# Kernel tuning notes

Hardware: AMD Instinct MI355X
Metric: run time of the kernel (lower is better)

Reference implementation:

```python
import jax, jax.numpy as jnp
import numpy as np

B, S, H = 8, 2048, 1024   # batch, seq, hidden_size
E = 4                     # num_experts (world_size=1 -> all local)
C = 1024                  # kv_cache_size (cache_decrement=0 -> uniform pyramid)
R = 4                     # LoRA rank
ALPHA = 1.0
TOP_K = 2
TEMP = 1.0
KEEP = C // 2             # pyramid compressor keeps top-half by importance


def _lora(z, A, Bm):
    # LoRALayer: (z @ A) @ B scaled by alpha/rank
    return (z @ A) @ Bm * (ALPHA / A.shape[-1])


def setup_inputs() -> dict:
    key = jax.random.key(0)
    ks = jax.random.split(key, 24)
    w = lambda k, shp: jax.random.normal(k, shp, jnp.float32) * 0.02
    return {
        'x': jax.random.normal(ks[0], (B, S, H), jnp.float32),
        'query': jax.random.normal(ks[1], (B, S, H), jnp.float32),
        'Wg': w(ks[2], (H, E)), 'bg': jnp.zeros((E,), jnp.float32),
        'Wq': w(ks[3], (H, H)), 'bq': jnp.zeros((H,), jnp.float32),
        'Wk': w(ks[4], (H, H)), 'bk': jnp.zeros((H,), jnp.float32),
        'Aq': w(ks[5], (H, R)), 'Bq': w(ks[6], (R, H)),
        'Ak': w(ks[7], (H, R)), 'Bk': w(ks[8], (R, H)),
        'We': w(ks[9], (E, H, H)), 'be': jnp.zeros((E, H), jnp.float32),
        'Ae': w(ks[10], (E, H, R)), 'Be': w(ks[11], (E, R, H)),
        'Av': w(ks[12], (E, H, R)), 'Bv': w(ks[13], (E, R, H)),
        'cache_keys': jax.random.normal(ks[14], (E, C, H), jnp.float32),
        'cache_values': jax.random.normal(ks[15], (E, C, H), jnp.float32),
        'cache_imp': jax.random.uniform(ks[16], (E, C), jnp.float32),
    }


def reference(x, query, Wg, bg, Wq, bq, Wk, bk, Aq, Bq, Ak, Bk,
              We, be, Ae, Be, Av, Bv, cache_keys, cache_values, cache_imp):
    # ---- AdaptiveRouter: softmax gate, top-2 renormalized, load-balance loss ----
    probs = jax.nn.softmax((x @ Wg + bg) / TEMP, axis=-1)             # [B,S,E]
    tw, ti = jax.lax.top_k(probs, TOP_K)                              # [B,S,K]
    twn = tw / tw.sum(-1, keepdims=True)
    onehot = jax.nn.one_hot(ti, E, dtype=x.dtype)                     # [B,S,K,E]
    routing = jnp.einsum('bsk,bske->bse', twn, onehot)                # [B,S,E]
    lb_loss = E * jnp.sum(probs.mean((0, 1)) * onehot.mean((0, 1, 2)))

    # ---- compute_token_importance (query provided): LoRA-augmented q/k attention ----
    q = query @ Wq + bq + _lora(query, Aq, Bq)
    k = x @ Wk + bk + _lora(x, Ak, Bk)
    att = jax.nn.softmax(jnp.einsum('bqh,bkh->bqk', q, k) / np.sqrt(H).astype(np.float32), axis=-1)
    importance = att.sum(axis=1)                                      # [B,S] column sums

    # ---- per-expert LoRA forward + pyramid-compressed cache read ----
    def expert_fn(We_i, be_i, Ae_i, Be_i, Av_i, Bv_i, cv_i, ci_i):
        eo = x @ We_i + be_i + _lora(x, Ae_i, Be_i)                   # [B,S,H]
        idx = jax.lax.top_k(ci_i, KEEP)[1]                            # keep top-half by importance
        vals = cv_i[idx]                                              # [KEEP,H] irregular gather
        vals = vals + _lora(vals, Av_i, Bv_i)                         # value LoRA on compressed cache
        return eo + jax.lax.stop_gradient(vals.mean(0))               # cached values are detached

    outs = jax.vmap(expert_fn)(We, be, Ae, Be, Av, Bv, cache_values, cache_imp)  # [E,B,S,H]
    expert_output = jnp.einsum('ebsh,bse->bsh', outs, routing)

    # ---- cache update at ptr=0 (detached buffer mutation -> returned new state) ----
    sg = jax.lax.stop_gradient
    new_keys = cache_keys.at[:, 0].set(jnp.broadcast_to(sg(x.mean((0, 1))), (E, H)))
    new_values = cache_values.at[:, 0].set(sg(outs.mean((1, 2))))
    new_imp = cache_imp.at[:, 0].set(sg(importance.mean()))
    return expert_output, lb_loss, new_keys, new_values, new_imp
```

## Files before the change

kernel.cpp:

```cpp
#include <hip/hip_runtime.h>

constexpr int kH    = 1024;
constexpr int kNT   = 16384;
constexpr int kE    = 4;
constexpr int kC    = 1024;
constexpr int kR    = 4;
constexpr int kKeep = 512;
constexpr float kLoraScale = 0.25f;
constexpr int kCapTiles = 136;
constexpr int kCapRows  = kCapTiles * 128;
constexpr int kNB      = kNT / 256;

constexpr size_t WS_RW     = 0;
constexpr size_t WS_G      = 65536;
constexpr size_t WS_XSUM   = 393216;
constexpr size_t WS_SHADOW = 394240;
constexpr size_t WS_TU     = 394752;
constexpr size_t WS_VBAR   = 394784;
constexpr size_t WS_FX     = 398880;
constexpr size_t WS_NEWV0  = 402976;
constexpr size_t WS_MSK    = 407072;
constexpr size_t WS_GBASE  = 411168;
constexpr size_t WS_BHIST  = 411176;
constexpr size_t WS_BOFF   = 411560;
constexpr size_t WS_RTPID  = 411944;
constexpr size_t WS_TPID   = 412088;
constexpr size_t WS_GRO    = 428472;
constexpr size_t WS_PERM   = 444856;
constexpr size_t WS_WCAT   = 462264;
constexpr size_t WS_AEXT   = 482744;
constexpr size_t WS_AEXTG  = 744888;
constexpr size_t WS_BEXT   = 1023416;
constexpr size_t WS_WET    = 1039800;
constexpr size_t WS_XG     = 3136952;

constexpr size_t OUT_LB = 16777216;
constexpr size_t OUT_NK = 16777217;

typedef __attribute__((ext_vector_type(8))) short bf16x8;
typedef __attribute__((ext_vector_type(4))) float f32x4;

__device__ __forceinline__ float wred(float v) {
#pragma unroll
  for (int off = 32; off; off >>= 1) v += __shfl_xor(v, off);
  return v;
}

__device__ __forceinline__ ushort f2bf(float f) {
  unsigned int u = __float_as_uint(f);
  u += 0x7FFFu + ((u >> 16) & 1u);
  return (ushort)(u >> 16);
}

__device__ __forceinline__ void gload16(const ushort* g, ushort* l) {
  __builtin_amdgcn_global_load_lds(
      (const __attribute__((address_space(1))) unsigned int*)g,
      (__attribute__((address_space(3))) unsigned int*)l, 16, 0, 0);
}

__device__ __forceinline__ int pid_a(int pid) { return pid < 3 ? 0 : (pid < 5 ? 1 : 2); }
__device__ __forceinline__ int pid_b(int pid) { return pid < 3 ? pid + 1 : (pid < 5 ? pid - 1 : 3); }

__global__ __launch_bounds__(256) void prep_k(const float* __restrict__ Wg,
                                              const float* __restrict__ Ae,
                                              const float* __restrict__ ci,
                                              float* __restrict__ wcat,
                                              float* __restrict__ msk) {
  __shared__ float imp[kC];
  const int b = blockIdx.x, tid = threadIdx.x;
  if (b < 80) {
    const int idx = b * 256 + tid;
    const int c = idx >> 10, k = idx & 1023;
    float v;
    if (c < 4) v = Wg[(size_t)k * 4 + c];
    else {
      const int e = (c - 4) >> 2, r = (c - 4) & 3;
      v = Ae[((size_t)e * kH + k) * kR + r];
    }
    wcat[(size_t)c * kH + k] = v;
  } else {
    const int e = (b - 80) >> 2, part = (b - 80) & 3;
    const int c = part * 256 + tid;
    for (int i = tid; i < kC; i += 256) imp[i] = ci[(size_t)e * kC + i];
    __syncthreads();
    const float v = imp[c];
    int rank = 0;
    for (int c2 = 0; c2 < kC; ++c2) {
      const float v2 = imp[c2];
      rank += (v2 > v) || (v2 == v && c2 < c);
    }
    msk[(size_t)e * kC + c] = (rank < kKeep) ? 1.0f : 0.0f;
  }
}

__global__ __launch_bounds__(256) void router_gemm_k(
    const float* __restrict__ x, const float* __restrict__ wcat,
    float* __restrict__ G) {
  __shared__ float xs_l[128][64];
  __shared__ float wt_l[20][64];
  const int tid = threadIdx.x;
  const int t0 = blockIdx.x * 128;
  const int tok = tid & 127, half = tid >> 7, cb = half * 10;
  float acc[10] = {};
  for (int kc = 0; kc < 16; ++kc) {
#pragma unroll
    for (int i = 0; i < 8; ++i) {
      const int idx = tid + i * 256;
      const int stok = idx >> 4, sslot = idx & 15;
      const float4 v =
          *(const float4*)(x + (size_t)(t0 + stok) * kH + kc * 64 + sslot * 4);
      *(float4*)&xs_l[stok][((sslot + stok) & 15) * 4] = v;
    }
    for (int idx = tid; idx < 320; idx += 256) {
      const int c = idx >> 4, slot = idx & 15;
      *(float4*)&wt_l[c][slot * 4] =
          *(const float4*)(wcat + (size_t)c * kH + kc * 64 + slot * 4);
    }
    __syncthreads();
#pragma unroll
    for (int k4 = 0; k4 < 16; ++k4) {
      const float4 xv = *(const float4*)&xs_l[tok][((k4 + tok) & 15) * 4];
#pragma unroll
      for (int j = 0; j < 10; ++j) {
        const float4 wv = *(const float4*)&wt_l[cb + j][k4 * 4];
        acc[j] += xv.x * wv.x + xv.y * wv.y + xv.z * wv.z + xv.w * wv.w;
      }
    }
    __syncthreads();
  }
#pragma unroll
  for (int j = 0; j < 10; ++j)
    G[(size_t)(cb + j) * kNT + t0 + tok] = acc[j];
}

__global__ __launch_bounds__(256) void router_fin_k(
    const float* __restrict__ G, const float* __restrict__ bg,
    float* __restrict__ rw, float* __restrict__ shadow,
    int* __restrict__ tpid, int* __restrict__ bhist,
    ushort* __restrict__ aext) {
  __shared__ float swacc[8];
  __shared__ int ihist[6];
  const int tid = threadIdx.x;
  const int t = blockIdx.x * 256 + tid;
  const int lane = tid & 63;
  if (tid < 8) swacc[tid] = 0.f;
  if (tid < 6) ihist[tid] = 0;
  __syncthreads();
  float lg[kE];
#pragma unroll
  for (int e = 0; e < kE; ++e) lg[e] = G[(size_t)e * kNT + t] + bg[e];
  float la[kE][kR];
#pragma unroll
  for (int e = 0; e < kE; ++e)
#pragma unroll
    for (int r = 0; r < kR; ++r)
      la[e][r] = G[(size_t)(4 + e * 4 + r) * kNT + t];
  const float mx = fmaxf(fmaxf(lg[0], lg[1]), fmaxf(lg[2], lg[3]));
  float ex[kE], se = 0.f;
#pragma unroll
  for (int e = 0; e < kE; ++e) { ex[e] = __expf(lg[e] - mx); se += ex[e]; }
  float pr[kE];
#pragma unroll
  for (int e = 0; e < kE; ++e) pr[e] = ex[e] / se;
  int e1 = 0;
#pragma unroll
  for (int e = 1; e < kE; ++e) if (pr[e] > pr[e1]) e1 = e;
  int e2 = (e1 == 0) ? 1 : 0;
#pragma unroll
  for (int e = 0; e < kE; ++e) if (e != e1 && pr[e] > pr[e2]) e2 = e;
  const float s2 = pr[e1] + pr[e2];
  float rwv[kE] = {0.f, 0.f, 0.f, 0.f};
  rwv[e1] = pr[e1] / s2; rwv[e2] = pr[e2] / s2;
  *(float4*)(rw + (size_t)t * kE) = make_float4(rwv[0], rwv[1], rwv[2], rwv[3]);
  const int lo = min(e1, e2), hi = max(e1, e2);
  const int pid = (lo == 0) ? hi - 1 : ((lo == 1) ? hi + 1 : 5);
  tpid[t] = pid;
  __align__(16) ushort o[32];
#pragma unroll
  for (int e = 0; e < kE; ++e) o[e] = f2bf(rwv[e]);
#pragma unroll
  for (int e = 0; e < kE; ++e)
#pragma unroll
    for (int r = 0; r < kR; ++r)
      o[4 + e * 4 + r] = f2bf(kLoraScale * rwv[e] * la[e][r]);
#pragma unroll
  for (int i = 20; i < 32; ++i) o[i] = 0;
#pragma unroll
  for (int q = 0; q < 4; ++q)
    *(float4*)&aext[(size_t)t * 32 + q * 8] = *(float4*)&o[q * 8];
  float vals[8];
#pragma unroll
  for (int e = 0; e < kE; ++e) {
    vals[e] = pr[e];
    vals[4 + e] = ((e == e1) ? 1.f : 0.f) + ((e == e2) ? 1.f : 0.f);
  }
#pragma unroll
  for (int j = 0; j < 8; ++j) {
    vals[j] = wred(vals[j]);
    if (lane == 0) atomicAdd(&swacc[j], vals[j]);
  }
  atomicAdd(&ihist[pid], 1);
  __syncthreads();
  if (tid < 8) atomicAdd(&shadow[(blockIdx.x & 63) * 8 + tid], swacc[tid]);
  if (tid < 6) bhist[blockIdx.x * 6 + tid] = ihist[tid];
}

__global__ __launch_bounds__(256) void colsum_k(const float* __restrict__ x,
                                                float* __restrict__ xsum) {
  const int rg = blockIdx.x, tid = threadIdx.x;
  const float* xp = x + (size_t)rg * 64 * kH + tid * 4;
  float s0 = 0.f, s1 = 0.f, s2 = 0.f, s3 = 0.f;
  for (int r = 0; r < 64; ++r) {
    const float4 v = *(const float4*)(xp + (size_t)r * kH);
    s0 += v.x; s1 += v.y; s2 += v.z; s3 += v.w;
  }
  atomicAdd(&xsum[tid * 4 + 0], s0);
  atomicAdd(&xsum[tid * 4 + 1], s1);
  atomicAdd(&xsum[tid * 4 + 2], s2);
  atomicAdd(&xsum[tid * 4 + 3], s3);
}

__global__ __launch_bounds__(256) void pscan_k(const int* __restrict__ bhist,
                                               int* __restrict__ gbase,
                                               int* __restrict__ boff,
                                               int* __restrict__ rtpid,
                                               int* __restrict__ perm) {
  __shared__ int pcnt_s[6];
  const int tid = threadIdx.x;
  if (tid < 6) {
    int run = 0;
    for (int b = 0; b < kNB; ++b) {
      boff[b * 6 + tid] = run;
      run += bhist[b * 6 + tid];
    }
    pcnt_s[tid] = run;
  }
  __syncthreads();
  if (tid == 0) {
    int base = 0;
    for (int g = 0; g < 6; ++g) {
      gbase[g] = base;
      const int tiles = (pcnt_s[g] + 127) >> 7;
      for (int ti = 0; ti < tiles; ++ti) rtpid[(base >> 7) + ti] = g;
      base += tiles << 7;
    }
    for (int i = base >> 7; i < kCapTiles; ++i) rtpid[i] = -1;
  }
  __syncthreads();
  if (tid < 6) {
    const int gb = gbase[tid];
    for (int b = 0; b < kNB; ++b) boff[b * 6 + tid] += gb;
  }
  for (int i = tid; i < kCapRows; i += 256) perm[i] = -1;
}

__global__ __launch_bounds__(256) void slot_k(const int* __restrict__ tpid,
                                              const int* __restrict__ boff,
                                              int* __restrict__ gro,
                                              int* __restrict__ perm) {
  __shared__ int wcnt[4][6];
  const int tid = threadIdx.x, w = tid >> 6, lane = tid & 63;
  const int t = blockIdx.x * 256 + tid;
  const int pid = tpid[t];
  unsigned long long mymask = 0;
  int cnt[6];
#pragma unroll
  for (int g = 0; g < 6; ++g) {
    const unsigned long long m = __ballot(pid == g);
    cnt[g] = __popcll(m);
    if (g == pid) mymask = m;
  }
  if (lane < 6) wcnt[w][lane] = cnt[lane];
  const int rank_in_wave =
      __popcll(mymask & ((lane == 63) ? 0x7FFFFFFFFFFFFFFFULL
                                      : ((1ULL << lane) - 1ULL)));
  __syncthreads();
  int base = 0;
  for (int w2 = 0; w2 < w; ++w2) base += wcnt[w2][pid];
  const int grow = boff[blockIdx.x * 6 + pid] + base + rank_in_wave;
  gro[t] = grow;
  perm[grow] = t;
}

__global__ __launch_bounds__(256) void xg_k(
    const float* __restrict__ x, const float* __restrict__ rw,
    const int* __restrict__ tpid, const ushort* __restrict__ aext,
    const int* __restrict__ gro, ushort* __restrict__ xg,
    ushort* __restrict__ aextg) {
  const int wave = threadIdx.x >> 6, lane = threadIdx.x & 63;
  const int t = blockIdx.x * 4 + wave;
  const int pid = tpid[t];
  const int grow = gro[t];
  const float wa = rw[(size_t)t * 4 + pid_a(pid)];
  const float wb = rw[(size_t)t * 4 + pid_b(pid)];
#pragma unroll
  for (int q = 0; q < 4; ++q) {
    const int c = q * 256 + lane * 4;
    const float4 v = *(const float4*)(x + (size_t)t * kH + c);
    ushort4 ua, ub;
    ua.x = f2bf(wa * v.x); ua.y = f2bf(wa * v.y);
    ua.z = f2bf(wa * v.z); ua.w = f2bf(wa * v.w);
    ub.x = f2bf(wb * v.x); ub.y = f2bf(wb * v.y);
    ub.z = f2bf(wb * v.z); ub.w = f2bf(wb * v.w);
    *(ushort4*)(xg + (size_t)grow * 2048 + c) = ua;
    *(ushort4*)(xg + (size_t)grow * 2048 + 1024 + c) = ub;
  }
  if (lane < 4)
    *(float4*)&aextg[(size_t)grow * 32 + lane * 8] =
        *(const float4*)&aext[(size_t)t * 32 + lane * 8];
}

__global__ __launch_bounds__(256) void wet_k(const float* __restrict__ We,
                                             ushort* __restrict__ wet) {
  __shared__ ushort tile[64][72];
  const int jb = blockIdx.x, kb = blockIdx.y, e = blockIdx.z;
  const int tid = threadIdx.x;
  const int rr = tid >> 4, cq = tid & 15;
#pragma unroll
  for (int p = 0; p < 4; ++p) {
    const int k = kb * 64 + p * 16 + rr;
    const float4 v = *(const float4*)&We[((size_t)e * kH + k) * kH + jb * 64 + cq * 4];
    tile[p * 16 + rr][cq * 4 + 0] = f2bf(v.x);
    tile[p * 16 + rr][cq * 4 + 1] = f2bf(v.y);
    tile[p * 16 + rr][cq * 4 + 2] = f2bf(v.z);
    tile[p * 16 + rr][cq * 4 + 3] = f2bf(v.w);
  }
  __syncthreads();
#pragma unroll
  for (int p = 0; p < 4; ++p) {
    const int j = jb * 64 + p * 16 + rr;
    ushort4 u;
    u.x = tile[cq * 4 + 0][p * 16 + rr];
    u.y = tile[cq * 4 + 1][p * 16 + rr];
    u.z = tile[cq * 4 + 2][p * 16 + rr];
    u.w = tile[cq * 4 + 3][p * 16 + rr];
    *(ushort4*)&wet[((size_t)e * kH + j) * kH + kb * 64 + cq * 4] = u;
  }
}

__global__ __launch_bounds__(256) void vbar_acc_k(const float* __restrict__ cv,
                                                  const float* __restrict__ msk,
                                                  float* __restrict__ vbar) {
  const int e = blockIdx.x, rc = blockIdx.y;
  const int tid = threadIdx.x;
  const float* base = cv + (size_t)e * kC * kH + (size_t)rc * 32 * kH + tid * 4;
  const float* m = msk + (size_t)e * kC + rc * 32;
  float s0 = 0.f, s1 = 0.f, s2 = 0.f, s3 = 0.f;
#pragma unroll 8
  for (int r = 0; r < 32; ++r) {
    const float mr = m[r];
    const float4 v = *(const float4*)(base + (size_t)r * kH);
    s0 += mr * v.x; s1 += mr * v.y; s2 += mr * v.z; s3 += mr * v.w;
  }
  const float sc = 1.0f / kKeep;
  atomicAdd(&vbar[(size_t)e * kH + tid * 4 + 0], s0 * sc);
  atomicAdd(&vbar[(size_t)e * kH + tid * 4 + 1], s1 * sc);
  atomicAdd(&vbar[(size_t)e * kH + tid * 4 + 2], s2 * sc);
  atomicAdd(&vbar[(size_t)e * kH + tid * 4 + 3], s3 * sc);
}

__global__ __launch_bounds__(256) void fx_acc_k(const float* __restrict__ We,
                                                const float* __restrict__ xsum,
                                                float* __restrict__ fx) {
  const int e = blockIdx.x, kc = blockIdx.y;
  const int tid = threadIdx.x;
  const float* Wb = We + (size_t)e * kH * kH + (size_t)kc * 64 * kH + tid * 4;
  const float* xs = xsum + kc * 64;
  float s0 = 0.f, s1 = 0.f, s2 = 0.f, s3 = 0.f;
#pragma unroll 8
  for (int k = 0; k < 64; ++k) {
    const float xm = xs[k] * (1.0f / kNT);
    const float4 v = *(const float4*)(Wb + (size_t)k * kH);
    s0 += xm * v.x; s1 += xm * v.y; s2 += xm * v.z; s3 += xm * v.w;
  }
  atomicAdd(&fx[(size_t)e * kH + tid * 4 + 0], s0);
  atomicAdd(&fx[(size_t)e * kH + tid * 4 + 1], s1);
  atomicAdd(&fx[(size_t)e * kH + tid * 4 + 2], s2);
  atomicAdd(&fx[(size_t)e * kH + tid * 4 + 3], s3);
}

__global__ __launch_bounds__(256) void tufin_k(
    const float* __restrict__ vbar, const float* __restrict__ xsum,
    const float* __restrict__ Av, const float* __restrict__ Ae,
    const float* __restrict__ be, const float* __restrict__ Bv,
    const float* __restrict__ Bee, const float* __restrict__ fx,
    float* __restrict__ newv0_ws, ushort* __restrict__ bext) {
  __shared__ float red[256];
  __shared__ float tus[8];
  const int e = blockIdx.x, tid = threadIdx.x;
  float p[8] = {};
#pragma unroll
  for (int q = 0; q < 4; ++q) {
    const int h = tid * 4 + q;
    const float vb = vbar[(size_t)e * kH + h];
    const float xm = xsum[h] * (1.0f / kNT);
    const float4 av = *(const float4*)(Av + ((size_t)e * kH + h) * kR);
    const float4 ae = *(const float4*)(Ae + ((size_t)e * kH + h) * kR);
    p[0] += vb * av.x; p[1] += vb * av.y; p[2] += vb * av.z; p[3] += vb * av.w;
    p[4] += xm * ae.x; p[5] += xm * ae.y; p[6] += xm * ae.z; p[7] += xm * ae.w;
  }
#pragma unroll
  for (int j = 0; j < 8; ++j) {
    red[tid] = p[j]; __syncthreads();
    for (int s2 = 128; s2; s2 >>= 1) {
      if (tid < s2) red[tid] += red[tid + s2];
      __syncthreads();
    }
    if (tid == 0) tus[j] = red[0];
    __syncthreads();
  }
  float t_[4], u_[4];
#pragma unroll
  for (int r = 0; r < kR; ++r) { t_[r] = tus[r]; u_[r] = tus[4 + r]; }
#pragma unroll
  for (int q = 0; q < 4; ++q) {
    const int col = q * 256 + tid;
    float lv = 0.f, le = 0.f;
#pragma unroll
    for (int r = 0; r < kR; ++r) {
      lv += t_[r] * Bv[((size_t)e * kR + r) * kH + col];
      le += u_[r] * Bee[((size_t)e * kR + r) * kH + col];
    }
    const float mv = vbar[(size_t)e * kH + col] + kLoraScale * lv;
    const float bias = be[(size_t)e * kH + col] + mv;
    newv0_ws[(size_t)e * kH + col] = fx[(size_t)e * kH + col] + kLoraScale * le + bias;
    bext[(size_t)col * 32 + e] = f2bf(bias);
#pragma unroll
    for (int r = 0; r < kR; ++r)
      bext[(size_t)col * 32 + 4 + e * 4 + r] =
          f2bf(Bee[((size_t)e * kR + r) * kH + col]);
    if (e == 0)
#pragma unroll
      for (int i = 20; i < 32; ++i) bext[(size_t)col * 32 + i] = 0;
  }
}

__global__ __launch_bounds__(256, 3) void moe_gemm_pair_k(
    const ushort* __restrict__ xg, const ushort* __restrict__ wet,
    const ushort* __restrict__ aextg, const ushort* __restrict__ bext,
    const int* __restrict__ rtpid, const int* __restrict__ perm,
    float* __restrict__ out) {
  const int bid = blockIdx.x;
  const int gid = (bid & 7) * 136 + (bid >> 3);
  const int rt = gid >> 3, ct = gid & 7;
  const int pid = rtpid[rt];
  if (pid < 0) return;
  __shared__ __align__(16) ushort As[3][128 * 32];
  __shared__ __align__(16) ushort Bs[3][128 * 32];
  __shared__ int perm_s[128];
  const int tid = threadIdx.x;
  const int lane = tid & 63, wave = tid >> 6;
  const int wm = wave >> 1, wn = wave & 1;
  const int r0 = rt * 128, c0 = ct * 128;
  const int ea = pid_a(pid), eb = pid_b(pid);
  if (tid < 128) perm_s[tid] = perm[r0 + tid];

  const int srow = lane >> 2;
  const int sslot = lane & 3;

  auto stage = [&](int buf, int kt) {
#pragma unroll
    for (int i = 0; i < 2; ++i) {
      const int j0 = wave * 32 + i * 16;
      const int r = j0 + srow;
      const int slot = sslot ^ ((r >> 1) & 3);
      const ushort* srcA;
      const ushort* srcB;
      if (kt < 64) {
        const int e = (kt < 32) ? ea : eb;
        const int ko = ((kt & 31) * 32) + ((kt < 32) ? 0 : 1024);
        srcA = xg + (size_t)(r0 + r) * 2048 + ko + slot * 8;
        srcB = wet + ((size_t)e * kH + c0 + r) * kH + (kt & 31) * 32 + slot * 8;
      } else {
        srcA = aextg + (size_t)(r0 + r) * 32 + slot * 8;
        srcB = bext + (size_t)(c0 + r) * 32 + slot * 8;
      }
      gload16(srcA, &As[buf][j0 * 32]);
      gload16(srcB, &Bs[buf][j0 * 32]);
    }
  };

  f32x4 acc[4][4] = {};
  stage(0, 0);
  stage(1, 1);
  asm volatile("s_waitcnt vmcnt(4)" ::: "memory");
  __builtin_amdgcn_sched_barrier(0);
  __builtin_amdgcn_s_barrier();

  const int rA = lane & 15;
  const int fslot = lane >> 4;
  int cur = 0, prev = 2;
  for (int kt = 0; kt <= 64; ++kt) {
    if (kt + 2 <= 64) stage(prev, kt + 2);
    bf16x8 a[4], b[4];
#pragma unroll
    for (int m = 0; m < 4; ++m) {
      const int r = wm * 64 + m * 16 + rA;
      const int sl = fslot ^ ((r >> 1) & 3);
      a[m] = *(const bf16x8*)&As[cur][r * 32 + sl * 8];
    }
#pragma unroll
    for (int n = 0; n < 4; ++n) {
      const int r = wn * 64 + n * 16 + rA;
      const int sl = fslot ^ ((r >> 1) & 3);
      b[n] = *(const bf16x8*)&Bs[cur][r * 32 + sl * 8];
    }
#pragma unroll
    for (int m = 0; m < 4; ++m)
#pragma unroll
      for (int n = 0; n < 4; ++n)
        acc[m][n] = __builtin_amdgcn_mfma_f32_16x16x32_bf16(a[m], b[n], acc[m][n], 0, 0, 0);
    if (kt < 64) {
      if (kt < 63) {
        asm volatile("s_waitcnt vmcnt(4)" ::: "memory");
      } else {
        asm volatile("s_waitcnt vmcnt(0)" ::: "memory");
      }
      __builtin_amdgcn_sched_barrier(0);
      __builtin_amdgcn_s_barrier();
    }
    prev = cur;
    cur = (cur == 2) ? 0 : cur + 1;
  }

#pragma unroll
  for (int m = 0; m < 4; ++m) {
#pragma unroll
    for (int v = 0; v < 4; ++v) {
      const int rl = wm * 64 + m * 16 + (lane >> 4) * 4 + v;
      const int tok = perm_s[rl];
      if (tok >= 0) {
        float* orow = out + (size_t)tok * kH + c0 + wn * 64 + (lane & 15);
#pragma unroll
        for (int n = 0; n < 4; ++n) orow[n * 16] = acc[m][n][v];
      }
    }
  }
}

__global__ __launch_bounds__(256) void copyfix_k(
    const float* __restrict__ ck, const float* __restrict__ cv,
    const float* __restrict__ ci, const float* __restrict__ xsum,
    const float* __restrict__ newv0, const float* __restrict__ shadow,
    float* __restrict__ out) {
  const size_t NK = (size_t)kE * kC * kH;
  const size_t idx = (size_t)blockIdx.x * 256 + threadIdx.x;
  if (idx < NK) {
    const size_t c = (idx >> 10) & (kC - 1), h = idx & (kH - 1);
    out[OUT_NK + idx] = (c == 0) ? xsum[h] * (1.0f / kNT) : ck[idx];
  } else if (idx < 2 * NK) {
    const size_t j = idx - NK;
    const size_t e = j >> 20, c = (j >> 10) & (kC - 1), h = j & (kH - 1);
    out[OUT_NK + idx] = (c == 0) ? newv0[e * kH + h] : cv[j];
  } else if (idx < 2 * NK + (size_t)kE * kC) {
    const size_t j = idx - 2 * NK;
    out[OUT_NK + idx] = ((j & (kC - 1)) == 0) ? 1.0f : ci[j];
  } else if (idx == 2 * NK + (size_t)kE * kC) {
    float lb = 0.f;
#pragma unroll
    for (int e = 0; e < kE; ++e) {
      float ps = 0.f, cn = 0.f;
      for (int s2 = 0; s2 < 64; ++s2) {
        ps += shadow[s2 * 8 + e];
        cn += shadow[s2 * 8 + 4 + e];
      }
      lb += (ps * (1.0f / kNT)) * (cn * (1.0f / (kNT * 2.0f)));
    }
    out[OUT_LB] = kE * lb;
  }
}

extern "C" void kernel_launch(void* const* d_in, const int* in_sizes, int n_in,
                              void* d_out, int out_size, void* d_ws, size_t ws_size,
                              hipStream_t stream) {
  const float* x   = (const float*)d_in[0];
  const float* Wg  = (const float*)d_in[2];
  const float* bg  = (const float*)d_in[3];
  const float* We  = (const float*)d_in[12];
  const float* be  = (const float*)d_in[13];
  const float* Ae  = (const float*)d_in[14];
  const float* Bee = (const float*)d_in[15];
  const float* Av  = (const float*)d_in[16];
  const float* Bv  = (const float*)d_in[17];
  const float* ck  = (const float*)d_in[18];
  const float* cv  = (const float*)d_in[19];
  const float* ci  = (const float*)d_in[20];
  float* ws  = (float*)d_ws;
  float* out = (float*)d_out;

  int* tpid  = (int*)(ws + WS_TPID);
  int* bhist = (int*)(ws + WS_BHIST);
  int* boff  = (int*)(ws + WS_BOFF);
  int* gbase = (int*)(ws + WS_GBASE);
  int* rtpid = (int*)(ws + WS_RTPID);
  int* gro   = (int*)(ws + WS_GRO);
  int* perm  = (int*)(ws + WS_PERM);
  ushort* aext  = (ushort*)(ws + WS_AEXT);
  ushort* aextg = (ushort*)(ws + WS_AEXTG);
  ushort* bext  = (ushort*)(ws + WS_BEXT);
  ushort* wet   = (ushort*)(ws + WS_WET);
  ushort* xg    = (ushort*)(ws + WS_XG);

  hipMemsetAsync(ws + WS_XSUM, 0, 9760 * sizeof(float), stream);
  prep_k<<<96, 256, 0, stream>>>(Wg, Ae, ci, ws + WS_WCAT, ws + WS_MSK);
  colsum_k<<<256, 256, 0, stream>>>(x, ws + WS_XSUM);
  router_gemm_k<<<kNT / 128, 256, 0, stream>>>(x, ws + WS_WCAT, ws + WS_G);
  router_fin_k<<<kNB, 256, 0, stream>>>(ws + WS_G, bg, ws + WS_RW,
                                        ws + WS_SHADOW, tpid, bhist, aext);
  pscan_k<<<1, 256, 0, stream>>>(bhist, gbase, boff, rtpid, perm);
  slot_k<<<kNB, 256, 0, stream>>>(tpid, boff, gro, perm);
  xg_k<<<kNT / 4, 256, 0, stream>>>(x, ws + WS_RW, tpid, aext, gro, xg, aextg);
  wet_k<<<dim3(16, 16, 4), 256, 0, stream>>>(We, wet);
  vbar_acc_k<<<dim3(kE, 32), 256, 0, stream>>>(cv, ws + WS_MSK, ws + WS_VBAR);
  fx_acc_k<<<dim3(kE, 16), 256, 0, stream>>>(We, ws + WS_XSUM, ws + WS_FX);
  tufin_k<<<kE, 256, 0, stream>>>(ws + WS_VBAR, ws + WS_XSUM, Av, Ae, be, Bv,
                                  Bee, ws + WS_FX, ws + WS_NEWV0, bext);
  moe_gemm_pair_k<<<kCapTiles * 8, 256, 0, stream>>>(
      xg, wet, aextg, bext, rtpid, perm, out);
  copyfix_k<<<32785, 256, 0, stream>>>(ck, cv, ci, ws + WS_XSUM, ws + WS_NEWV0,
                                       ws + WS_SHADOW, out);
}
```

Measured before the change: 381.2 us.

## Fuse column sum into router GEMM, fx into We transpose; double-buffer MoE GEMM

The token column sum of x is now computed inside the router GEMM from its shared-memory tile, which removes a separate 64MB read of x. The We·xmean product is folded into the We transpose/convert kernel, so the separate fx pass over We goes away. The MoE GEMM moves from a three-stage to a two-stage shared-memory pipeline with full waits and syncthreads, targeting two blocks per CU instead of three. This costs latency hiding in the main GEMM and adds extra atomics.

Result: slower. 703.6 us (+84.6%).

```diff
diff --git a/kernel.cpp b/kernel.cpp
--- a/kernel.cpp
+++ b/kernel.cpp
@@ -95,12 +95,14 @@
 
 __global__ __launch_bounds__(256) void router_gemm_k(
     const float* __restrict__ x, const float* __restrict__ wcat,
-    float* __restrict__ G) {
+    float* __restrict__ G, float* __restrict__ xsum) {
   __shared__ float xs_l[128][64];
   __shared__ float wt_l[20][64];
+  __shared__ float cs_l[4][64];
   const int tid = threadIdx.x;
   const int t0 = blockIdx.x * 128;
   const int tok = tid & 127, half = tid >> 7, cb = half * 10;
+  const int cc = tid & 63, crg = tid >> 6;
   float acc[10] = {};
   for (int kc = 0; kc < 16; ++kc) {
 #pragma unroll
@@ -126,7 +128,17 @@
         acc[j] += xv.x * wv.x + xv.y * wv.y + xv.z * wv.z + xv.w * wv.w;
       }
     }
+    float csp = 0.f;
+#pragma unroll 8
+    for (int i = 0; i < 32; ++i) {
+      const int r = crg * 32 + i;
+      csp += xs_l[r][(((cc >> 2) + r) & 15) * 4 + (cc & 3)];
+    }
+    cs_l[crg][cc] = csp;
     __syncthreads();
+    if (tid < 64)
+      atomicAdd(&xsum[kc * 64 + tid],
+                cs_l[0][tid] + cs_l[1][tid] + cs_l[2][tid] + cs_l[3][tid]);
   }
 #pragma unroll
   for (int j = 0; j < 10; ++j)
@@ -205,21 +217,6 @@
   if (tid < 6) bhist[blockIdx.x * 6 + tid] = ihist[tid];
 }
 
-__global__ __launch_bounds__(256) void colsum_k(const float* __restrict__ x,
-                                                float* __restrict__ xsum) {
-  const int rg = blockIdx.x, tid = threadIdx.x;
-  const float* xp = x + (size_t)rg * 64 * kH + tid * 4;
-  float s0 = 0.f, s1 = 0.f, s2 = 0.f, s3 = 0.f;
-  for (int r = 0; r < 64; ++r) {
-    const float4 v = *(const float4*)(xp + (size_t)r * kH);
-    s0 += v.x; s1 += v.y; s2 += v.z; s3 += v.w;
-  }
-  atomicAdd(&xsum[tid * 4 + 0], s0);
-  atomicAdd(&xsum[tid * 4 + 1], s1);
-  atomicAdd(&xsum[tid * 4 + 2], s2);
-  atomicAdd(&xsum[tid * 4 + 3], s3);
-}
-
 __global__ __launch_bounds__(256) void pscan_k(const int* __restrict__ bhist,
                                                int* __restrict__ gbase,
                                                int* __restrict__ boff,
@@ -311,11 +308,18 @@
 }
 
 __global__ __launch_bounds__(256) void wet_k(const float* __restrict__ We,
-                                             ushort* __restrict__ wet) {
+                                             const float* __restrict__ xsum,
+                                             ushort* __restrict__ wet,
+                                             float* __restrict__ fx) {
   __shared__ ushort tile[64][72];
+  __shared__ float fxl[16][64];
+  __shared__ float xml[64];
   const int jb = blockIdx.x, kb = blockIdx.y, e = blockIdx.z;
   const int tid = threadIdx.x;
   const int rr = tid >> 4, cq = tid & 15;
+  if (tid < 64) xml[tid] = xsum[kb * 64 + tid] * (1.0f / kNT);
+  __syncthreads();
+  float fxp[4] = {};
 #pragma unroll
   for (int p = 0; p < 4; ++p) {
     const int k = kb * 64 + p * 16 + rr;
@@ -324,8 +328,17 @@
     tile[p * 16 + rr][cq * 4 + 1] = f2bf(v.y);
     tile[p * 16 + rr][cq * 4 + 2] = f2bf(v.z);
     tile[p * 16 + rr][cq * 4 + 3] = f2bf(v.w);
-  }
-  __syncthreads();
+    const float xm = xml[p * 16 + rr];
+    fxp[0] += xm * v.x; fxp[1] += xm * v.y; fxp[2] += xm * v.z; fxp[3] += xm * v.w;
+  }
+  *(float4*)&fxl[rr][cq * 4] = make_float4(fxp[0], fxp[1], fxp[2], fxp[3]);
+  __syncthreads();
+  if (tid < 64) {
+    float s = 0.f;
+#pragma unroll
+    for (int r2 = 0; r2 < 16; ++r2) s += fxl[r2][tid];
+    atomicAdd(&fx[(size_t)e * kH + jb * 64 + tid], s);
+  }
 #pragma unroll
   for (int p = 0; p < 4; ++p) {
     const int j = jb * 64 + p * 16 + rr;
@@ -359,26 +372,6 @@
   atomicAdd(&vbar[(size_t)e * kH + tid * 4 + 3], s3 * sc);
 }
 
-__global__ __launch_bounds__(256) void fx_acc_k(const float* __restrict__ We,
-                                                const float* __restrict__ xsum,
-                                                float* __restrict__ fx) {
-  const int e = blockIdx.x, kc = blockIdx.y;
-  const int tid = threadIdx.x;
-  const float* Wb = We + (size_t)e * kH * kH + (size_t)kc * 64 * kH + tid * 4;
-  const float* xs = xsum + kc * 64;
-  float s0 = 0.f, s1 = 0.f, s2 = 0.f, s3 = 0.f;
-#pragma unroll 8
-  for (int k = 0; k < 64; ++k) {
-    const float xm = xs[k] * (1.0f / kNT);
-    const float4 v = *(const float4*)(Wb + (size_t)k * kH);
-    s0 += xm * v.x; s1 += xm * v.y; s2 += xm * v.z; s3 += xm * v.w;
-  }
-  atomicAdd(&fx[(size_t)e * kH + tid * 4 + 0], s0);
-  atomicAdd(&fx[(size_t)e * kH + tid * 4 + 1], s1);
-  atomicAdd(&fx[(size_t)e * kH + tid * 4 + 2], s2);
-  atomicAdd(&fx[(size_t)e * kH + tid * 4 + 3], s3);
-}
-
 __global__ __launch_bounds__(256) void tufin_k(
     const float* __restrict__ vbar, const float* __restrict__ xsum,
     const float* __restrict__ Av, const float* __restrict__ Ae,
@@ -435,7 +428,7 @@
   }
 }
 
-__global__ __launch_bounds__(256, 3) void moe_gemm_pair_k(
+__global__ __launch_bounds__(256, 2) void moe_gemm_pair_k(
     const ushort* __restrict__ xg, const ushort* __restrict__ wet,
     const ushort* __restrict__ aextg, const ushort* __restrict__ bext,
     const int* __restrict__ rtpid, const int* __restrict__ perm,
@@ -445,8 +438,8 @@
   const int rt = gid >> 3, ct = gid & 7;
   const int pid = rtpid[rt];
   if (pid < 0) return;
-  __shared__ __align__(16) ushort As[3][128 * 32];
-  __shared__ __align__(16) ushort Bs[3][128 * 32];
+  __shared__ __align__(16) ushort As[2][128 * 32];
+  __shared__ __align__(16) ushort Bs[2][128 * 32];
   __shared__ int perm_s[128];
   const int tid = threadIdx.x;
   const int lane = tid & 63, wave = tid >> 6;
@@ -482,45 +475,35 @@
 
   f32x4 acc[4][4] = {};
   stage(0, 0);
-  stage(1, 1);
-  asm volatile("s_waitcnt vmcnt(4)" ::: "memory");
-  __builtin_amdgcn_sched_barrier(0);
-  __builtin_amdgcn_s_barrier();
+  asm volatile("s_waitcnt vmcnt(0)" ::: "memory");
+  __syncthreads();
 
   const int rA = lane & 15;
   const int fslot = lane >> 4;
-  int cur = 0, prev = 2;
+  int buf = 0;
   for (int kt = 0; kt <= 64; ++kt) {
-    if (kt + 2 <= 64) stage(prev, kt + 2);
+    if (kt < 64) stage(buf ^ 1, kt + 1);
     bf16x8 a[4], b[4];
 #pragma unroll
     for (int m = 0; m < 4; ++m) {
       const int r = wm * 64 + m * 16 + rA;
       const int sl = fslot ^ ((r >> 1) & 3);
-      a[m] = *(const bf16x8*)&As[cur][r * 32 + sl * 8];
+      a[m] = *(const bf16x8*)&As[buf][r * 32 + sl * 8];
     }
 #pragma unroll
     for (int n = 0; n < 4; ++n) {
       const int r = wn * 64 + n * 16 + rA;
       const int sl = fslot ^ ((r >> 1) & 3);
-      b[n] = *(const bf16x8*)&Bs[cur][r * 32 + sl * 8];
+      b[n] = *(const bf16x8*)&Bs[buf][r * 32 + sl * 8];
     }
 #pragma unroll
     for (int m = 0; m < 4; ++m)
 #pragma unroll
       for (int n = 0; n < 4; ++n)
         acc[m][n] = __builtin_amdgcn_mfma_f32_16x16x32_bf16(a[m], b[n], acc[m][n], 0, 0, 0);
-    if (kt < 64) {
-      if (kt < 63) {
-        asm volatile("s_waitcnt vmcnt(4)" ::: "memory");
-      } else {
-        asm volatile("s_waitcnt vmcnt(0)" ::: "memory");
-      }
-      __builtin_amdgcn_sched_barrier(0);
-      __builtin_amdgcn_s_barrier();
-    }
-    prev = cur;
-    cur = (cur == 2) ? 0 : cur + 1;
+    if (kt < 64) asm volatile("s_waitcnt vmcnt(0)" ::: "memory");
+    __syncthreads();
+    buf ^= 1;
   }
 
 #pragma unroll
@@ -603,16 +586,16 @@
 
   hipMemsetAsync(ws + WS_XSUM, 0, 9760 * sizeof(float), stream);
   prep_k<<<96, 256, 0, stream>>>(Wg, Ae, ci, ws + WS_WCAT, ws + WS_MSK);
-  colsum_k<<<256, 256, 0, stream>>>(x, ws + WS_XSUM);
-  router_gemm_k<<<kNT / 128, 256, 0, stream>>>(x, ws + WS_WCAT, ws + WS_G);
+  router_gemm_k<<<kNT / 128, 256, 0, stream>>>(x, ws + WS_WCAT, ws + WS_G,
+                                               ws + WS_XSUM);
   router_fin_k<<<kNB, 256, 0, stream>>>(ws + WS_G, bg, ws + WS_RW,
                                         ws + WS_SHADOW, tpid, bhist, aext);
   pscan_k<<<1, 256, 0, stream>>>(bhist, gbase, boff, rtpid, perm);
   slot_k<<<kNB, 256, 0, stream>>>(tpid, boff, gro, perm);
   xg_k<<<kNT / 4, 256, 0, stream>>>(x, ws + WS_RW, tpid, aext, gro, xg, aextg);
-  wet_k<<<dim3(16, 16, 4), 256, 0, stream>>>(We, wet);
+  wet_k<<<dim3(16, 16, 4), 256, 0, stream>>>(We, ws + WS_XSUM, wet,
+                                             ws + WS_FX);
   vbar_acc_k<<<dim3(kE, 32), 256, 0, stream>>>(cv, ws + WS_MSK, ws + WS_VBAR);
-  fx_acc_k<<<dim3(kE, 16), 256, 0, stream>>>(We, ws + WS_XSUM, ws + WS_FX);
   tufin_k<<<kE, 256, 0, stream>>>(ws + WS_VBAR, ws + WS_XSUM, Av, Ae, be, Bv,
                                   Bee, ws + WS_FX, ws + WS_NEWV0, bext);
   moe_gemm_pair_k<<<kCapTiles * 8, 256, 0, stream>>>(
```
